# Kernel tuning notes

Hardware: AMD Instinct MI355X
Metric: run time of the kernel (lower is better)

The kernel has to match this reference:

```python
import jax, jax.numpy as jnp
import numpy as np

PAD_IDX = 1  # word2vec key_to_index['<PAD>'] / padding_idx in the original
VOCAB, EMBED, HIDDEN, SEQ = 100000, 300, 512, 1024


def setup_inputs() -> dict:
    key = jax.random.key(0)
    k = jax.random.split(key, 8)
    s = 1.0 / np.sqrt(HIDDEN)  # PyTorch LSTM init scale
    return {
        "input_seq": jax.random.randint(k[0], (1, SEQ), 0, VOCAB, dtype=jnp.int64)
                     if jax.config.jax_enable_x64 else
                     jax.random.randint(k[0], (1, SEQ), 0, VOCAB, dtype=jnp.int32),
        "h0": jnp.zeros((1, 1, HIDDEN), jnp.float32),
        "c0": jnp.zeros((1, 1, HIDDEN), jnp.float32),
        "emb": jax.random.normal(k[1], (VOCAB, EMBED), jnp.float32),  # frozen word2vec table
        "W_ih": jax.random.uniform(k[2], (4 * HIDDEN, EMBED), jnp.float32, -s, s),
        "W_hh": jax.random.uniform(k[3], (4 * HIDDEN, HIDDEN), jnp.float32, -s, s),
        "b_ih": jax.random.uniform(k[4], (4 * HIDDEN,), jnp.float32, -s, s),
        "b_hh": jax.random.uniform(k[5], (4 * HIDDEN,), jnp.float32, -s, s),
    }


def _lstm_scan(xs, is_pad, h, c, W_ih, W_hh, b_ih, b_hh):
    # xs: [S, E]; PAD steps leave (h, c, out) untouched, matching the `continue`.
    x_gates = xs @ W_ih.T + b_ih  # [S, 4H] -- hoist input projection out of the scan
    H = h.shape[-1]

    def step(carry, inp):
        h, c, out = carry
        xg, pad = inp
        g = xg + h @ W_hh.T + b_hh                 # [4H], PyTorch gate order i,f,g,o
        i, f, gg, o = jnp.split(g, 4)
        c_new = jax.nn.sigmoid(f) * c + jax.nn.sigmoid(i) * jnp.tanh(gg)
        h_new = jax.nn.sigmoid(o) * jnp.tanh(c_new)
        h = jnp.where(pad, h, h_new)
        c = jnp.where(pad, c, c_new)
        out = jnp.where(pad, out, h_new)
        return (h, c, out), None

    (h, c, out), _ = jax.lax.scan(step, (h, c, jnp.zeros(H, xs.dtype)), (x_gates, is_pad))
    return h, c, out


def reference(input_seq, h0, c0, emb, W_ih, W_hh, b_ih, b_hh):
    tokens = input_seq[0]                 # batch==1 in the original
    xs = emb[tokens]                      # [S, E] embedding gather (fused into recurrence)
    is_pad = tokens == PAD_IDX
    h, c, out = _lstm_scan(xs, is_pad, h0[0, 0], c0[0, 0], W_ih, W_hh, b_ih, b_hh)
    # original returns output=None if every token is PAD; here out stays zeros.
    return (out[None, None, :], (h[None, None, :], c[None, None, :]))
```

## Files before the change

kernel.cpp:

```cpp
#include <hip/hip_runtime.h>
#include <math.h>

#define SEQ    1024
#define EMBED  300
#define HIDDEN 512
#define G4     2048
#define NB     128
#define NBLK   256
#define TPB    256
#define UPB    (HIDDEN/NB)
#define PAD_IDX 1
#define SENT   0x7FC00BADu

#define HSLOT  32
#define HROW   (NB * HSLOT)

__device__ float        g_xg[SEQ * G4];
__device__ float        g_hp[(SEQ + 1) * HROW];
__device__ unsigned int g_done;
__device__ float        g_sink;

__device__ __forceinline__ float sigmoidf_(float x) {
    return 1.f / (1.f + __expf(-x));
}
__device__ __forceinline__ float tanhf_(float x) {
    return 1.f - 2.f / (__expf(2.f * x) + 1.f);
}

#define DPP_ADD(v, ctrl)                                                      \
    (v) += __int_as_float(__builtin_amdgcn_update_dpp(                        \
        0, __float_as_int(v), (ctrl), 0xf, 0xf, true))

__global__ __launch_bounds__(256) void xgates_kernel(
    const int* __restrict__ seq, const float* __restrict__ h0,
    const float* __restrict__ emb, const float* __restrict__ W_ih,
    const float* __restrict__ b_ih, const float* __restrict__ b_hh)
{
    const int bx = blockIdx.x, tid = threadIdx.x;

    if (bx == 0 && tid == 0) g_done = 0u;
    for (int i = bx * 256 + tid; i < (SEQ + 1) * HROW; i += 256 * 256) {
        int step = i >> 12, slot = i & (HROW - 1);
        int blk = slot >> 5, k = slot & (HSLOT - 1);
        float v = __uint_as_float(SENT);
        if (step == 0 && k < UPB) v = h0[blk * UPB + k];
        g_hp[i] = v;
    }

    const int t_tile = bx >> 1, k_half = bx & 1;
    const int t0 = t_tile * 8;

    __shared__ int tok_s[8];
    __shared__ __align__(16) float embt[8][304];

    if (tid < 8) tok_s[tid] = seq[t0 + tid];
    __syncthreads();
    for (int idx = tid; idx < 8 * EMBED; idx += 256) {
        int tt = idx / EMBED;
        int e  = idx - tt * EMBED;
        embt[tt][e] = emb[(size_t)tok_s[tt] * EMBED + e];
    }
    __syncthreads();

    const int kbase = k_half * 1024 + tid;
    const float4* wr0 = (const float4*)(W_ih + (size_t)(kbase      ) * EMBED);
    const float4* wr1 = (const float4*)(W_ih + (size_t)(kbase + 256) * EMBED);
    const float4* wr2 = (const float4*)(W_ih + (size_t)(kbase + 512) * EMBED);
    const float4* wr3 = (const float4*)(W_ih + (size_t)(kbase + 768) * EMBED);

    float acc[4][8];
    #pragma unroll
    for (int kk = 0; kk < 4; kk++)
        #pragma unroll
        for (int tt = 0; tt < 8; tt++) acc[kk][tt] = 0.f;

    for (int e4 = 0; e4 < EMBED / 4; e4++) {
        float4 em[8];
        #pragma unroll
        for (int tt = 0; tt < 8; tt++)
            em[tt] = *(const float4*)&embt[tt][e4 * 4];
        float4 w[4];
        w[0] = wr0[e4]; w[1] = wr1[e4]; w[2] = wr2[e4]; w[3] = wr3[e4];
        #pragma unroll
        for (int kk = 0; kk < 4; kk++) {
            #pragma unroll
            for (int tt = 0; tt < 8; tt++) {
                float a = acc[kk][tt];
                a = fmaf(w[kk].x, em[tt].x, a);
                a = fmaf(w[kk].y, em[tt].y, a);
                a = fmaf(w[kk].z, em[tt].z, a);
                a = fmaf(w[kk].w, em[tt].w, a);
                acc[kk][tt] = a;
            }
        }
    }
    #pragma unroll
    for (int kk = 0; kk < 4; kk++) {
        int k = kbase + kk * 256;
        float bias = b_ih[k] + b_hh[k];
        #pragma unroll
        for (int tt = 0; tt < 8; tt++)
            g_xg[(size_t)(t0 + tt) * G4 + k] = acc[kk][tt] + bias;
    }
}

__global__ __launch_bounds__(TPB, 1) void lstm_kernel(
    const int* __restrict__ seq, const float* __restrict__ h0,
    const float* __restrict__ c0, const float* __restrict__ Whh,
    float* __restrict__ out)
{
    const int b = blockIdx.x, tid = threadIdx.x;

    if (b >= NB) {
        if (tid < 128) {
            float a0 = 1.0f + tid, a1 = 2.0f, a2 = 3.0f, a3 = 4.0f;
            for (;;) {
                #pragma unroll
                for (int i = 0; i < 128; i++) {
                    a0 = fmaf(a0, 1.000001f, 0.5f);
                    a1 = fmaf(a1, 0.999999f, 0.25f);
                    a2 = fmaf(a2, 1.0000005f, a0);
                    a3 = fmaf(a3, 0.9999995f, a1);
                }
                if (__hip_atomic_load(&g_done, __ATOMIC_RELAXED,
                                      __HIP_MEMORY_SCOPE_AGENT)) break;
            }
            if (a0 == 1234.5678f && a1 == a2) g_sink = a3;
        }
        return;
    }

    const int u = tid >> 6;
    const int lane = tid & 63;
    const int g = lane >> 4, c = lane & 15;
    const int R = g * HIDDEN + b * UPB + u;

    const float* wrow = Whh + (size_t)R * HIDDEN + c * 32;
    float4 wreg[8];
    #pragma unroll
    for (int i = 0; i < 8; i++) {
        int off = (4 * i + 4 * c) & 31;
        wreg[i] = *(const float4*)(wrow + off);
    }

    __shared__ __align__(16) float h_lds[2][HIDDEN];
    __shared__ int tok_lds[SEQ];

    for (int i = tid; i < SEQ; i += TPB) tok_lds[i] = seq[i];

    const bool owner = (lane == 0);
    const bool gate_lane = (c == 0);
    float c_state = 0.f, h_state = 0.f;
    if (owner) {
        c_state = c0[b * UPB + u];
        h_state = h0[b * UPB + u];
    }
    __syncthreads();

    int np = 0;
    bool any = false;

    for (int t = 0; t < SEQ; t++) {
        int tok = tok_lds[t];
        if (tok == PAD_IDX) continue;
        any = true;

        float xgv = 0.f;
        if (gate_lane) {
            xgv = g_xg[(size_t)t * G4 + g * HIDDEN + b * UPB + u];
        }

        if (tid < NB) {
            const unsigned long long* hb = (const unsigned long long*)
                (g_hp + (size_t)np * HROW + tid * HSLOT);
            unsigned long long p0, p1;
            for (;;) {
                p0 = __hip_atomic_load(hb + 0, __ATOMIC_RELAXED,
                                       __HIP_MEMORY_SCOPE_AGENT);
                p1 = __hip_atomic_load(hb + 1, __ATOMIC_RELAXED,
                                       __HIP_MEMORY_SCOPE_AGENT);
                if ((unsigned)p0 != SENT && (unsigned)(p0 >> 32) != SENT &&
                    (unsigned)p1 != SENT && (unsigned)(p1 >> 32) != SENT)
                    break;
            }
            unsigned long long* dst =
                (unsigned long long*)&h_lds[np & 1][tid * UPB];
            dst[0] = p0; dst[1] = p1;
        }
        __syncthreads();

        const float* hc = h_lds[np & 1] + c * 32;
        float4 a4 = {0.f, 0.f, 0.f, 0.f};
        #pragma unroll
        for (int i = 0; i < 8; i++) {
            int off = (4 * i + 4 * c) & 31;
            float4 h4 = *(const float4*)(hc + off);
            a4.x = fmaf(wreg[i].x, h4.x, a4.x);
            a4.y = fmaf(wreg[i].y, h4.y, a4.y);
            a4.z = fmaf(wreg[i].z, h4.z, a4.z);
            a4.w = fmaf(wreg[i].w, h4.w, a4.w);
        }
        float dotv = (a4.x + a4.y) + (a4.z + a4.w);
        DPP_ADD(dotv, 0xB1);
        DPP_ADD(dotv, 0x4E);
        DPP_ADD(dotv, 0x141);
        DPP_ADD(dotv, 0x140);

        float act = 0.f;
        if (gate_lane) {
            float z = xgv + dotv;
            act = (g == 2) ? tanhf_(z) : sigmoidf_(z);
        }
        float fv = __shfl(act, 16);
        float gv = __shfl(act, 32);
        float ov = __shfl(act, 48);

        if (owner) {
            c_state = fv * c_state + act * gv;
            h_state = ov * tanhf_(c_state);
            __hip_atomic_store(
                (unsigned*)(g_hp + (size_t)(np + 1) * HROW + b * HSLOT) + u,
                __float_as_uint(h_state),
                __ATOMIC_RELAXED, __HIP_MEMORY_SCOPE_AGENT);
        }
        np++;
    }

    if (owner) {
        int uo = b * UPB + u;
        out[uo]              = any ? h_state : 0.f;
        out[HIDDEN + uo]     = h_state;
        out[2 * HIDDEN + uo] = c_state;
    }
    if (b == 0 && tid == 0) {
        __hip_atomic_store(&g_done, 1u, __ATOMIC_RELAXED,
                           __HIP_MEMORY_SCOPE_AGENT);
    }
}

extern "C" void kernel_launch(void* const* d_in, const int* in_sizes, int n_in,
                              void* d_out, int out_size, void* d_ws, size_t ws_size,
                              hipStream_t stream)
{
    const int*   seq  = (const int*)  d_in[0];
    const float* h0   = (const float*)d_in[1];
    const float* c0   = (const float*)d_in[2];
    const float* emb  = (const float*)d_in[3];
    const float* W_ih = (const float*)d_in[4];
    const float* W_hh = (const float*)d_in[5];
    const float* b_ih = (const float*)d_in[6];
    const float* b_hh = (const float*)d_in[7];
    float* out = (float*)d_out;

    hipLaunchKernelGGL(xgates_kernel, dim3(256), dim3(256), 0, stream,
                       seq, h0, emb, W_ih, b_ih, b_hh);

    void* args[] = { (void*)&seq, (void*)&h0, (void*)&c0, (void*)&W_hh,
                     (void*)&out };
    hipLaunchCooperativeKernel((const void*)lstm_kernel, dim3(NBLK), dim3(TPB),
                               args, 0, stream);
}
```

Measured before the change: 1.831 ms.

## Poll hidden state per wave directly from global, drop LDS barrier and padding

Each wave now polls the full 512-float hidden vector straight from the global exchange buffer, 8 floats per lane, instead of having 128 threads poll padded slots and stage them through LDS with a block-wide __syncthreads. The exchange rows are packed densely (slot of 4 instead of 32), and each lane computes all four gate dot products over its 8-element slice, reduced with DPP plus cross-row shuffles. This is meant to remove the per-step block barrier and the LDS round trip from the sequential critical path. In exchange every wave issues its own global polls, which adds memory traffic, and the reduction needs extra shuffles for four accumulators.

```diff
diff --git a/kernel.cpp b/kernel.cpp
--- a/kernel.cpp
+++ b/kernel.cpp
@@ -12,11 +12,11 @@
 #define PAD_IDX 1
 #define SENT   0x7FC00BADu
 
-#define HSLOT  32
+#define HSLOT  4
 #define HROW   (NB * HSLOT)
 
-__device__ float        g_xg[SEQ * G4];
-__device__ float        g_hp[(SEQ + 1) * HROW];
+__device__ __align__(128) float g_xg[SEQ * G4];
+__device__ __align__(128) float g_hp[(SEQ + 1) * HROW];
 __device__ unsigned int g_done;
 __device__ float        g_sink;
 
@@ -30,6 +30,19 @@
 #define DPP_ADD(v, ctrl)                                                      \
     (v) += __int_as_float(__builtin_amdgcn_update_dpp(                        \
         0, __float_as_int(v), (ctrl), 0xf, 0xf, true))
+#define DPP_ROW_REDUCE(v)                                                     \
+    do {                                                                      \
+        DPP_ADD(v, 0xB1);                   \
+        DPP_ADD(v, 0x4E);                   \
+        DPP_ADD(v, 0x141);                               \
+        DPP_ADD(v, 0x140);                                    \
+    } while (0)
+
+#define LDQ(p) __hip_atomic_load((p), __ATOMIC_RELAXED, __HIP_MEMORY_SCOPE_AGENT)
+
+__device__ __forceinline__ bool okq(unsigned long long q) {
+    return ((unsigned)q != SENT) & ((unsigned)(q >> 32) != SENT);
+}
 
 __global__ __launch_bounds__(256) void xgates_kernel(
     const int* __restrict__ seq, const float* __restrict__ h0,
@@ -40,10 +53,9 @@
 
     if (bx == 0 && tid == 0) g_done = 0u;
     for (int i = bx * 256 + tid; i < (SEQ + 1) * HROW; i += 256 * 256) {
-        int step = i >> 12, slot = i & (HROW - 1);
-        int blk = slot >> 5, k = slot & (HSLOT - 1);
+        int step = i >> 9, slot = i & (HROW - 1);
         float v = __uint_as_float(SENT);
-        if (step == 0 && k < UPB) v = h0[blk * UPB + k];
+        if (step == 0) v = h0[slot];
         g_hp[i] = v;
     }
 
@@ -132,28 +144,27 @@
 
     const int u = tid >> 6;
     const int lane = tid & 63;
-    const int g = lane >> 4, c = lane & 15;
-    const int R = g * HIDDEN + b * UPB + u;
-
-    const float* wrow = Whh + (size_t)R * HIDDEN + c * 32;
-    float4 wreg[8];
+    const int g = lane >> 4;
+    const int U = b * UPB + u;
+
+    float wv[4][8];
     #pragma unroll
-    for (int i = 0; i < 8; i++) {
-        int off = (4 * i + 4 * c) & 31;
-        wreg[i] = *(const float4*)(wrow + off);
-    }
-
-    __shared__ __align__(16) float h_lds[2][HIDDEN];
+    for (int gg = 0; gg < 4; gg++) {
+        const float* wr = Whh + (size_t)(gg * HIDDEN + U) * HIDDEN + lane * 8;
+        float4 wa = *(const float4*)wr;
+        float4 wb = *(const float4*)(wr + 4);
+        wv[gg][0] = wa.x; wv[gg][1] = wa.y; wv[gg][2] = wa.z; wv[gg][3] = wa.w;
+        wv[gg][4] = wb.x; wv[gg][5] = wb.y; wv[gg][6] = wb.z; wv[gg][7] = wb.w;
+    }
+
     __shared__ int tok_lds[SEQ];
-
     for (int i = tid; i < SEQ; i += TPB) tok_lds[i] = seq[i];
 
     const bool owner = (lane == 0);
-    const bool gate_lane = (c == 0);
     float c_state = 0.f, h_state = 0.f;
     if (owner) {
-        c_state = c0[b * UPB + u];
-        h_state = h0[b * UPB + u];
+        c_state = c0[U];
+        h_state = h0[U];
     }
     __syncthreads();
 
@@ -165,52 +176,51 @@
         if (tok == PAD_IDX) continue;
         any = true;
 
-        float xgv = 0.f;
-        if (gate_lane) {
-            xgv = g_xg[(size_t)t * G4 + g * HIDDEN + b * UPB + u];
-        }
-
-        if (tid < NB) {
-            const unsigned long long* hb = (const unsigned long long*)
-                (g_hp + (size_t)np * HROW + tid * HSLOT);
-            unsigned long long p0, p1;
-            for (;;) {
-                p0 = __hip_atomic_load(hb + 0, __ATOMIC_RELAXED,
-                                       __HIP_MEMORY_SCOPE_AGENT);
-                p1 = __hip_atomic_load(hb + 1, __ATOMIC_RELAXED,
-                                       __HIP_MEMORY_SCOPE_AGENT);
-                if ((unsigned)p0 != SENT && (unsigned)(p0 >> 32) != SENT &&
-                    (unsigned)p1 != SENT && (unsigned)(p1 >> 32) != SENT)
-                    break;
-            }
-            unsigned long long* dst =
-                (unsigned long long*)&h_lds[np & 1][tid * UPB];
-            dst[0] = p0; dst[1] = p1;
-        }
-        __syncthreads();
-
-        const float* hc = h_lds[np & 1] + c * 32;
-        float4 a4 = {0.f, 0.f, 0.f, 0.f};
-        #pragma unroll
-        for (int i = 0; i < 8; i++) {
-            int off = (4 * i + 4 * c) & 31;
-            float4 h4 = *(const float4*)(hc + off);
-            a4.x = fmaf(wreg[i].x, h4.x, a4.x);
-            a4.y = fmaf(wreg[i].y, h4.y, a4.y);
-            a4.z = fmaf(wreg[i].z, h4.z, a4.z);
-            a4.w = fmaf(wreg[i].w, h4.w, a4.w);
-        }
-        float dotv = (a4.x + a4.y) + (a4.z + a4.w);
-        DPP_ADD(dotv, 0xB1);
-        DPP_ADD(dotv, 0x4E);
-        DPP_ADD(dotv, 0x141);
-        DPP_ADD(dotv, 0x140);
-
-        float act = 0.f;
-        if (gate_lane) {
-            float z = xgv + dotv;
-            act = (g == 2) ? tanhf_(z) : sigmoidf_(z);
-        }
+        const unsigned long long* hb =
+            (const unsigned long long*)(g_hp + (size_t)np * HROW) + lane * 4;
+        unsigned long long q0 = LDQ(hb + 0);
+        unsigned long long q1 = LDQ(hb + 1);
+        unsigned long long q2 = LDQ(hb + 2);
+        unsigned long long q3 = LDQ(hb + 3);
+        float xgv = g_xg[(size_t)t * G4 + g * HIDDEN + U];
+        while (!(okq(q0) & okq(q1) & okq(q2) & okq(q3))) {
+            if (!okq(q0)) q0 = LDQ(hb + 0);
+            if (!okq(q1)) q1 = LDQ(hb + 1);
+            if (!okq(q2)) q2 = LDQ(hb + 2);
+            if (!okq(q3)) q3 = LDQ(hb + 3);
+        }
+
+        float h8[8];
+        h8[0] = __uint_as_float((unsigned)q0);
+        h8[1] = __uint_as_float((unsigned)(q0 >> 32));
+        h8[2] = __uint_as_float((unsigned)q1);
+        h8[3] = __uint_as_float((unsigned)(q1 >> 32));
+        h8[4] = __uint_as_float((unsigned)q2);
+        h8[5] = __uint_as_float((unsigned)(q2 >> 32));
+        h8[6] = __uint_as_float((unsigned)q3);
+        h8[7] = __uint_as_float((unsigned)(q3 >> 32));
+
+        float a0 = 0.f, a1 = 0.f, a2 = 0.f, a3 = 0.f;
+        #pragma unroll
+        for (int j = 0; j < 8; j++) {
+            float hv = h8[j];
+            a0 = fmaf(wv[0][j], hv, a0);
+            a1 = fmaf(wv[1][j], hv, a1);
+            a2 = fmaf(wv[2][j], hv, a2);
+            a3 = fmaf(wv[3][j], hv, a3);
+        }
+
+        DPP_ROW_REDUCE(a0); DPP_ROW_REDUCE(a1);
+        DPP_ROW_REDUCE(a2); DPP_ROW_REDUCE(a3);
+        a0 += __shfl_xor(a0, 16); a0 += __shfl_xor(a0, 32);
+        a1 += __shfl_xor(a1, 16); a1 += __shfl_xor(a1, 32);
+        a2 += __shfl_xor(a2, 16); a2 += __shfl_xor(a2, 32);
+        a3 += __shfl_xor(a3, 16); a3 += __shfl_xor(a3, 32);
+
+        float S = (g == 0) ? a0 : (g == 1) ? a1 : (g == 2) ? a2 : a3;
+        float z = xgv + S;
+        float act = (g == 2) ? tanhf_(z) : sigmoidf_(z);
+
         float fv = __shfl(act, 16);
         float gv = __shfl(act, 32);
         float ov = __shfl(act, 48);
@@ -219,7 +229,7 @@
             c_state = fv * c_state + act * gv;
             h_state = ov * tanhf_(c_state);
             __hip_atomic_store(
-                (unsigned*)(g_hp + (size_t)(np + 1) * HROW + b * HSLOT) + u,
+                (unsigned*)(g_hp + (size_t)(np + 1) * HROW) + U,
                 __float_as_uint(h_state),
                 __ATOMIC_RELAXED, __HIP_MEMORY_SCOPE_AGENT);
         }
@@ -227,10 +237,9 @@
     }
 
     if (owner) {
-        int uo = b * UPB + u;
-        out[uo]              = any ? h_state : 0.f;
-        out[HIDDEN + uo]     = h_state;
-        out[2 * HIDDEN + uo] = c_state;
+        out[U]              = any ? h_state : 0.f;
+        out[HIDDEN + U]     = h_state;
+        out[2 * HIDDEN + U] = c_state;
     }
     if (b == 0 && tid == 0) {
         __hip_atomic_store(&g_done, 1u, __ATOMIC_RELAXED,
```

Result: slower. 5.897 ms (+222.1%).

## Fuse input projection into cooperative LSTM kernel and overlap it with recurrence

Applied to the files above, without the earlier changes.

The separate input-projection kernel is merged into the cooperative recurrence kernel. After a grid sync that initializes buffers with sentinels, the otherwise idle blocks 128-255 compute the input-gate projections, which the recurrence blocks consume via spin-waiting on sentinel values. This removes a kernel launch and lets the projection overlap with the serial recurrence. It adds a grid-wide sync, a sentinel fill of the large xgate buffer, and per-step polling on xgate readiness.

```diff
diff --git a/kernel.cpp b/kernel.cpp
--- a/kernel.cpp
+++ b/kernel.cpp
@@ -1,4 +1,5 @@
 #include <hip/hip_runtime.h>
+#include <hip/hip_cooperative_groups.h>
 #include <math.h>
 
 #define SEQ    1024
@@ -15,8 +16,8 @@
 #define HSLOT  32
 #define HROW   (NB * HSLOT)
 
-__device__ float        g_xg[SEQ * G4];
-__device__ float        g_hp[(SEQ + 1) * HROW];
+__device__ __align__(128) float g_xg[SEQ * G4];
+__device__ __align__(128) float g_hp[(SEQ + 1) * HROW];
 __device__ unsigned int g_done;
 __device__ float        g_sink;
 
@@ -31,87 +32,96 @@
     (v) += __int_as_float(__builtin_amdgcn_update_dpp(                        \
         0, __float_as_int(v), (ctrl), 0xf, 0xf, true))
 
-__global__ __launch_bounds__(256) void xgates_kernel(
+#define LDA_U32(p) __hip_atomic_load((p), __ATOMIC_RELAXED, __HIP_MEMORY_SCOPE_AGENT)
+
+__global__ __launch_bounds__(TPB, 1) void fused_kernel(
     const int* __restrict__ seq, const float* __restrict__ h0,
-    const float* __restrict__ emb, const float* __restrict__ W_ih,
-    const float* __restrict__ b_ih, const float* __restrict__ b_hh)
+    const float* __restrict__ c0, const float* __restrict__ emb,
+    const float* __restrict__ W_ih, const float* __restrict__ Whh,
+    const float* __restrict__ b_ih, const float* __restrict__ b_hh,
+    float* __restrict__ out)
 {
-    const int bx = blockIdx.x, tid = threadIdx.x;
-
-    if (bx == 0 && tid == 0) g_done = 0u;
-    for (int i = bx * 256 + tid; i < (SEQ + 1) * HROW; i += 256 * 256) {
+    const int b = blockIdx.x, tid = threadIdx.x;
+    const int gid = b * TPB + tid;
+
+    if (gid == 0) g_done = 0u;
+    for (int i = gid; i < (SEQ + 1) * HROW; i += NBLK * TPB) {
         int step = i >> 12, slot = i & (HROW - 1);
         int blk = slot >> 5, k = slot & (HSLOT - 1);
         float v = __uint_as_float(SENT);
         if (step == 0 && k < UPB) v = h0[blk * UPB + k];
         g_hp[i] = v;
     }
-
-    const int t_tile = bx >> 1, k_half = bx & 1;
-    const int t0 = t_tile * 8;
-
-    __shared__ int tok_s[8];
-    __shared__ __align__(16) float embt[8][304];
-
-    if (tid < 8) tok_s[tid] = seq[t0 + tid];
-    __syncthreads();
-    for (int idx = tid; idx < 8 * EMBED; idx += 256) {
-        int tt = idx / EMBED;
-        int e  = idx - tt * EMBED;
-        embt[tt][e] = emb[(size_t)tok_s[tt] * EMBED + e];
-    }
-    __syncthreads();
-
-    const int kbase = k_half * 1024 + tid;
-    const float4* wr0 = (const float4*)(W_ih + (size_t)(kbase      ) * EMBED);
-    const float4* wr1 = (const float4*)(W_ih + (size_t)(kbase + 256) * EMBED);
-    const float4* wr2 = (const float4*)(W_ih + (size_t)(kbase + 512) * EMBED);
-    const float4* wr3 = (const float4*)(W_ih + (size_t)(kbase + 768) * EMBED);
-
-    float acc[4][8];
-    #pragma unroll
-    for (int kk = 0; kk < 4; kk++)
-        #pragma unroll
-        for (int tt = 0; tt < 8; tt++) acc[kk][tt] = 0.f;
-
-    for (int e4 = 0; e4 < EMBED / 4; e4++) {
-        float4 em[8];
-        #pragma unroll
-        for (int tt = 0; tt < 8; tt++)
-            em[tt] = *(const float4*)&embt[tt][e4 * 4];
-        float4 w[4];
-        w[0] = wr0[e4]; w[1] = wr1[e4]; w[2] = wr2[e4]; w[3] = wr3[e4];
-        #pragma unroll
-        for (int kk = 0; kk < 4; kk++) {
+    for (int i = gid; i < SEQ * G4; i += NBLK * TPB)
+        g_xg[i] = __uint_as_float(SENT);
+
+    cooperative_groups::this_grid().sync();
+
+    if (b >= NB) {
+        const int hb = b - NB;
+        __shared__ int tok_s[8];
+        __shared__ __align__(16) float embt[8][304];
+
+        for (int it = 0; it < 2; it++) {
+            const int item  = hb + it * NB;
+            const int t0    = (item >> 1) * 8;
+            const int k_half = item & 1;
+
+            if (tid < 8) tok_s[tid] = seq[t0 + tid];
+            __syncthreads();
+            for (int idx = tid; idx < 8 * EMBED; idx += TPB) {
+                int tt = idx / EMBED;
+                int e  = idx - tt * EMBED;
+                embt[tt][e] = emb[(size_t)tok_s[tt] * EMBED + e];
+            }
+            __syncthreads();
+
+            const int kbase = k_half * 1024 + tid;
+            const float4* wr0 = (const float4*)(W_ih + (size_t)(kbase      ) * EMBED);
+            const float4* wr1 = (const float4*)(W_ih + (size_t)(kbase + 256) * EMBED);
+            const float4* wr2 = (const float4*)(W_ih + (size_t)(kbase + 512) * EMBED);
+            const float4* wr3 = (const float4*)(W_ih + (size_t)(kbase + 768) * EMBED);
+
+            float acc[4][8];
             #pragma unroll
-            for (int tt = 0; tt < 8; tt++) {
-                float a = acc[kk][tt];
-                a = fmaf(w[kk].x, em[tt].x, a);
-                a = fmaf(w[kk].y, em[tt].y, a);
-                a = fmaf(w[kk].z, em[tt].z, a);
-                a = fmaf(w[kk].w, em[tt].w, a);
-                acc[kk][tt] = a;
-            }
-        }
-    }
-    #pragma unroll
-    for (int kk = 0; kk < 4; kk++) {
-        int k = kbase + kk * 256;
-        float bias = b_ih[k] + b_hh[k];
-        #pragma unroll
-        for (int tt = 0; tt < 8; tt++)
-            g_xg[(size_t)(t0 + tt) * G4 + k] = acc[kk][tt] + bias;
-    }
-}
-
-__global__ __launch_bounds__(TPB, 1) void lstm_kernel(
-    const int* __restrict__ seq, const float* __restrict__ h0,
-    const float* __restrict__ c0, const float* __restrict__ Whh,
-    float* __restrict__ out)
-{
-    const int b = blockIdx.x, tid = threadIdx.x;
-
-    if (b >= NB) {
+            for (int kk = 0; kk < 4; kk++)
+                #pragma unroll
+                for (int tt = 0; tt < 8; tt++) acc[kk][tt] = 0.f;
+
+            for (int e4 = 0; e4 < EMBED / 4; e4++) {
+                float4 em[8];
+                #pragma unroll
+                for (int tt = 0; tt < 8; tt++)
+                    em[tt] = *(const float4*)&embt[tt][e4 * 4];
+                float4 w[4];
+                w[0] = wr0[e4]; w[1] = wr1[e4]; w[2] = wr2[e4]; w[3] = wr3[e4];
+                #pragma unroll
+                for (int kk = 0; kk < 4; kk++) {
+                    #pragma unroll
+                    for (int tt = 0; tt < 8; tt++) {
+                        float a = acc[kk][tt];
+                        a = fmaf(w[kk].x, em[tt].x, a);
+                        a = fmaf(w[kk].y, em[tt].y, a);
+                        a = fmaf(w[kk].z, em[tt].z, a);
+                        a = fmaf(w[kk].w, em[tt].w, a);
+                        acc[kk][tt] = a;
+                    }
+                }
+            }
+            #pragma unroll
+            for (int kk = 0; kk < 4; kk++) {
+                int k = kbase + kk * 256;
+                float bias = b_ih[k] + b_hh[k];
+                #pragma unroll
+                for (int tt = 0; tt < 8; tt++) {
+                    __hip_atomic_store(&g_xg[(size_t)(t0 + tt) * G4 + k],
+                                       acc[kk][tt] + bias,
+                                       __ATOMIC_RELAXED, __HIP_MEMORY_SCOPE_AGENT);
+                }
+            }
+            __syncthreads();
+        }
+
         if (tid < 128) {
             float a0 = 1.0f + tid, a1 = 2.0f, a2 = 3.0f, a3 = 4.0f;
             for (;;) {
@@ -165,19 +175,19 @@
         if (tok == PAD_IDX) continue;
         any = true;
 
-        float xgv = 0.f;
-        if (gate_lane) {
-            xgv = g_xg[(size_t)t * G4 + g * HIDDEN + b * UPB + u];
-        }
+        const unsigned* xgp = (const unsigned*)&g_xg[(size_t)t * G4
+                                                     + g * HIDDEN + b * UPB + u];
+        unsigned xgu = 0u;
+        if (gate_lane) xgu = LDA_U32(xgp);
 
         if (tid < NB) {
-            const unsigned long long* hb = (const unsigned long long*)
-                (g_hp + (size_t)np * HROW + tid * HSLOT);
+            const unsigned long long* hb_ =
+                (const unsigned long long*)(g_hp + (size_t)np * HROW + tid * HSLOT);
             unsigned long long p0, p1;
             for (;;) {
-                p0 = __hip_atomic_load(hb + 0, __ATOMIC_RELAXED,
+                p0 = __hip_atomic_load(hb_ + 0, __ATOMIC_RELAXED,
                                        __HIP_MEMORY_SCOPE_AGENT);
-                p1 = __hip_atomic_load(hb + 1, __ATOMIC_RELAXED,
+                p1 = __hip_atomic_load(hb_ + 1, __ATOMIC_RELAXED,
                                        __HIP_MEMORY_SCOPE_AGENT);
                 if ((unsigned)p0 != SENT && (unsigned)(p0 >> 32) != SENT &&
                     (unsigned)p1 != SENT && (unsigned)(p1 >> 32) != SENT)
@@ -208,7 +218,8 @@
 
         float act = 0.f;
         if (gate_lane) {
-            float z = xgv + dotv;
+            while (xgu == SENT) xgu = LDA_U32(xgp);
+            float z = __uint_as_float(xgu) + dotv;
             act = (g == 2) ? tanhf_(z) : sigmoidf_(z);
         }
         float fv = __shfl(act, 16);
@@ -252,11 +263,9 @@
     const float* b_hh = (const float*)d_in[7];
     float* out = (float*)d_out;
 
-    hipLaunchKernelGGL(xgates_kernel, dim3(256), dim3(256), 0, stream,
-                       seq, h0, emb, W_ih, b_ih, b_hh);
-
-    void* args[] = { (void*)&seq, (void*)&h0, (void*)&c0, (void*)&W_hh,
+    void* args[] = { (void*)&seq, (void*)&h0, (void*)&c0, (void*)&emb,
+                     (void*)&W_ih, (void*)&W_hh, (void*)&b_ih, (void*)&b_hh,
                      (void*)&out };
-    hipLaunchCooperativeKernel((const void*)lstm_kernel, dim3(NBLK), dim3(TPB),
+    hipLaunchCooperativeKernel((const void*)fused_kernel, dim3(NBLK), dim3(TPB),
                                args, 0, stream);
 }
```

New measurement: 1.937 ms. 5.8% more time.
